# Optimization experiments

Hardware: AMD Instinct MI355X
Metric: run time of the kernel (lower is better)

The kernel has to match this reference:

```python
import jax, jax.numpy as jnp
import numpy as np


def _highway(x, Ws, bs):
    # Ws: [n_hw, 2H, H] (torch Linear layout), bs: [n_hw, 2H]
    H = x.shape[-1]
    for i in range(Ws.shape[0]):
        proj = jnp.einsum('bsh,oh->bso', x, Ws[i]) + bs[i]
        nonlin = jax.nn.relu(proj[..., :H])
        gate = jax.nn.sigmoid(proj[..., H:])
        x = gate * x + (1.0 - gate) * nonlin
    return x


def setup_inputs() -> dict:
    key = jax.random.key(0)
    ks = jax.random.split(key, 10)
    B, S, H, L, W, NHW = 32, 512, 512, 2, 4, 2
    scale = 1.0 / np.sqrt(H)
    return {
        'inputs': jax.random.normal(ks[0], (B, S, H), dtype=jnp.float32),
        'masks': jnp.ones((B, S), dtype=jnp.int32),
        'fwd_pads': jax.random.normal(ks[1], (L, W, H), dtype=jnp.float32) * scale,
        'bwd_pads': jax.random.normal(ks[2], (L, W, H), dtype=jnp.float32) * scale,
        'fwd_ws': jax.random.normal(ks[3], (L, W + 1), dtype=jnp.float32),
        'bwd_ws': jax.random.normal(ks[4], (L, W + 1), dtype=jnp.float32),
        'fwd_hw_W': jax.random.normal(ks[5], (L, NHW, 2 * H, H), dtype=jnp.float32) * scale,
        'fwd_hw_b': jax.random.normal(ks[6], (L, NHW, 2 * H), dtype=jnp.float32) * 0.1,
        'bwd_hw_W': jax.random.normal(ks[7], (L, NHW, 2 * H, H), dtype=jnp.float32) * scale,
        'bwd_hw_b': jax.random.normal(ks[8], (L, NHW, 2 * H), dtype=jnp.float32) * 0.1,
    }


def reference(inputs, masks, fwd_pads, bwd_pads, fwd_ws, bwd_ws,
              fwd_hw_W, fwd_hw_b, bwd_hw_W, bwd_hw_b):
    # inputs: [B,S,H]; masks unused (as in the torch module)
    B, S, H = inputs.shape
    L, W, _ = fwd_pads.shape
    fwd_in = inputs
    bwd_in = inputs
    outs = []
    for l in range(L):
        fp = jnp.broadcast_to(fwd_pads[l], (B, W, H))
        bp = jnp.broadcast_to(bwd_pads[l], (B, W, H))
        pf = jnp.concatenate([fp, fwd_in, bp], axis=1)  # [B, S+2W, H]
        pb = jnp.concatenate([fp, bwd_in, bp], axis=1)
        # forward window at t covers padded positions t..t+W (causal)
        f_win = jnp.stack([pf[:, k:k + S] for k in range(W + 1)], axis=0)  # [W+1,B,S,H]
        f_out = jnp.einsum('k,kbsh->bsh', fwd_ws[l], f_win)
        # backward window at t covers padded positions t+W..t+2W (anti-causal)
        b_win = jnp.stack([pb[:, W + k:W + k + S] for k in range(W + 1)], axis=0)
        b_out = jnp.einsum('k,kbsh->bsh', bwd_ws[l], b_win)
        f_out = _highway(f_out, fwd_hw_W[l], fwd_hw_b[l])
        b_out = _highway(b_out, bwd_hw_W[l], bwd_hw_b[l])
        fwd_in, bwd_in = f_out, b_out
        outs.append(jnp.concatenate([f_out, b_out], axis=-1))
    return jnp.stack(outs, axis=0)  # [L, B, S, 2H]
```

## Files before the change

kernel.cpp:

```cpp
#include <hip/hip_runtime.h>
#include <hip/hip_bf16.h>

typedef __attribute__((ext_vector_type(8))) short bf16x8;
typedef __attribute__((ext_vector_type(4))) float floatx4;

#define B_ 32
#define S_ 512
#define H_ 512
#define M_ (B_*S_)
#define K_ 512
#define N_ 1024

__device__ __forceinline__ void gload_lds16(const void* g, void* l) {
  __builtin_amdgcn_global_load_lds(
      (const __attribute__((address_space(1))) void*)g,
      (__attribute__((address_space(3))) void*)l, 16, 0, 0);
}

__global__ void cvt_kernel(const float* __restrict__ src,
                           __hip_bfloat16* __restrict__ dst, int n4) {
  int t = blockIdx.x * 256 + threadIdx.x;
  if (t >= n4) return;
  float4 v = *(const float4*)(src + (size_t)t * 4);
  union { ushort4 u; __hip_bfloat16 h[4]; } pk;
  pk.h[0] = __float2bfloat16(v.x);
  pk.h[1] = __float2bfloat16(v.y);
  pk.h[2] = __float2bfloat16(v.z);
  pk.h[3] = __float2bfloat16(v.w);
  *(ushort4*)((unsigned short*)dst + (size_t)t * 4) = pk.u;
}

__global__ void conv_kernel(const float* __restrict__ inf, const float* __restrict__ inb,
                            int instride,
                            const float* __restrict__ fpad, const float* __restrict__ bpad,
                            const float* __restrict__ fw, const float* __restrict__ bw,
                            __hip_bfloat16* __restrict__ xaf, __hip_bfloat16* __restrict__ xab) {
  int t = blockIdx.x * 256 + threadIdx.x;
  int dir = blockIdx.y;
  int row = t >> 7;
  int hv  = (t & 127) << 2;
  int s = row & (S_ - 1);
  float4 a = make_float4(0.f, 0.f, 0.f, 0.f);
  if (dir == 0) {
#pragma unroll
    for (int k = 0; k < 5; ++k) {
      float w = fw[k];
      const float* src = (s + k < 4) ? (fpad + (size_t)(s + k) * H_ + hv)
                                     : (inf + (size_t)(row + k - 4) * instride + hv);
      float4 v = *(const float4*)src;
      a.x += w * v.x; a.y += w * v.y; a.z += w * v.z; a.w += w * v.w;
    }
  } else {
#pragma unroll
    for (int k = 0; k < 5; ++k) {
      float w = bw[k];
      const float* src = (s + k < S_) ? (inb + (size_t)(row + k) * instride + hv)
                                      : (bpad + (size_t)(s + k - S_) * H_ + hv);
      float4 v = *(const float4*)src;
      a.x += w * v.x; a.y += w * v.y; a.z += w * v.z; a.w += w * v.w;
    }
  }
  __hip_bfloat16* xa = dir ? xab : xaf;
  union { ushort4 u; __hip_bfloat16 h[4]; } pk;
  pk.h[0] = __float2bfloat16(a.x);
  pk.h[1] = __float2bfloat16(a.y);
  pk.h[2] = __float2bfloat16(a.z);
  pk.h[3] = __float2bfloat16(a.w);
  *(ushort4*)((unsigned short*)xa + (size_t)row * H_ + hv) = pk.u;
}

__global__ __launch_bounds__(512, 2)
void hw_gemm(const __hip_bfloat16* __restrict__ Af, const __hip_bfloat16* __restrict__ Ab,
             const __hip_bfloat16* __restrict__ Wf, const __hip_bfloat16* __restrict__ Wb,
             const float* __restrict__ biasf, const float* __restrict__ biasb,
             __hip_bfloat16* __restrict__ Anf, __hip_bfloat16* __restrict__ Anb,
             float* __restrict__ outp, int final_mode) {
  __shared__ __align__(16) char smem[65536];

  const int tid = threadIdx.x;
  const int lane = tid & 63, wave = tid >> 6;
  const int wm = wave >> 1, wn = wave & 1;
  const int quad = lane >> 4, l16 = lane & 15;
  const int dir = blockIdx.z;

  const int n = blockIdx.x;
  const int by = n & 63, bx = n >> 6;
  const int m0 = by * 256;
  const int h0 = bx * 128;

  const __hip_bfloat16* A = dir ? Ab : Af;
  const __hip_bfloat16* Wm = dir ? Wb : Wf;
  const float* bias = dir ? biasb : biasf;
  __hip_bfloat16* An = dir ? Anb : Anf;

  floatx4 acc[4][8];
#pragma unroll
  for (int i = 0; i < 4; ++i)
#pragma unroll
    for (int j = 0; j < 8; ++j) acc[i][j] = (floatx4){0.f, 0.f, 0.f, 0.f};

  const int srow = lane >> 2;
  const int skk  = (((lane & 3) ^ ((lane >> 3) & 3)) << 3);
  const int key  = (l16 >> 1) & 3;
  const int xkp0 = bx * 4 + wn * 2;
  const int xkp1 = xkp0 + 1;

  const __hip_bfloat16* aptr[2];
  const __hip_bfloat16* bptr[2];
#pragma unroll
  for (int c = 0; c < 2; ++c) {
    const int chunk = wave * 2 + c;
    aptr[c] = A + (size_t)(m0 + chunk * 16 + srow) * K_ + skk;
    const int brow = chunk * 16 + srow;
    const int wnp = brow >> 7, rr = brow & 127;
    const int wrow = (rr < 64) ? (h0 + wnp * 64 + rr)
                               : (512 + h0 + wnp * 64 + (rr - 64));
    bptr[c] = Wm + (size_t)wrow * K_ + skk;
  }

#pragma unroll
  for (int c = 0; c < 2; ++c) {
    const int chunk = wave * 2 + c;
    gload_lds16(aptr[c], smem + chunk * 1024);
    gload_lds16(bptr[c], smem + 16384 + chunk * 1024);
  }
  __syncthreads();

  unsigned int xsp[4][4][2];
  int cur = 0;
  for (int kp = 0; kp < 16; ++kp) {
    const __hip_bfloat16* cA = (const __hip_bfloat16*)(smem + (cur << 15));
    const __hip_bfloat16* cB = (const __hip_bfloat16*)(smem + (cur << 15) + 16384);
    if (kp < 15) {
      char* nb = smem + ((cur ^ 1) << 15);
      const int kb = (kp + 1) * 32;
#pragma unroll
      for (int c = 0; c < 2; ++c) {
        const int chunk = wave * 2 + c;
        gload_lds16(aptr[c] + kb, nb + chunk * 1024);
        gload_lds16(bptr[c] + kb, nb + 16384 + chunk * 1024);
      }
    }
    if (kp == xkp0) {
      const unsigned short* pA = (const unsigned short*)cA;
#pragma unroll
      for (int i = 0; i < 4; ++i)
#pragma unroll
        for (int jj = 0; jj < 2; ++jj)
#pragma unroll
          for (int rh = 0; rh < 2; ++rh) {
            const int ra0 = wm * 64 + i * 16 + quad * 4 + rh * 2;
            const int ra1 = ra0 + 1;
            const int c2 = jj * 16 + l16;
            unsigned int lo = pA[ra0 * 32 + ((((c2 >> 3) ^ ((ra0 >> 1) & 3)) << 3) | (c2 & 7))];
            unsigned int hi = pA[ra1 * 32 + ((((c2 >> 3) ^ ((ra1 >> 1) & 3)) << 3) | (c2 & 7))];
            xsp[i][jj][rh] = lo | (hi << 16);
          }
    }
    if (kp == xkp1) {
      const unsigned short* pA = (const unsigned short*)cA;
#pragma unroll
      for (int i = 0; i < 4; ++i)
#pragma unroll
        for (int jj = 0; jj < 2; ++jj)
#pragma unroll
          for (int rh = 0; rh < 2; ++rh) {
            const int ra0 = wm * 64 + i * 16 + quad * 4 + rh * 2;
            const int ra1 = ra0 + 1;
            const int c2 = jj * 16 + l16;
            unsigned int lo = pA[ra0 * 32 + ((((c2 >> 3) ^ ((ra0 >> 1) & 3)) << 3) | (c2 & 7))];
            unsigned int hi = pA[ra1 * 32 + ((((c2 >> 3) ^ ((ra1 >> 1) & 3)) << 3) | (c2 & 7))];
            xsp[i][2 + jj][rh] = lo | (hi << 16);
          }
    }
    bf16x8 av[4];
#pragma unroll
    for (int i = 0; i < 4; ++i) {
      const int ra = wm * 64 + i * 16 + l16;
      av[i] = *(const bf16x8*)&cA[ra * 32 + ((quad ^ key) << 3)];
    }
#pragma unroll
    for (int jh = 0; jh < 2; ++jh) {
      bf16x8 bv[4];
#pragma unroll
      for (int jj = 0; jj < 4; ++jj) {
        const int rb = wn * 128 + (jh * 4 + jj) * 16 + l16;
        bv[jj] = *(const bf16x8*)&cB[rb * 32 + ((quad ^ key) << 3)];
      }
#pragma unroll
      for (int i = 0; i < 4; ++i)
#pragma unroll
        for (int jj = 0; jj < 4; ++jj)
          acc[i][jh * 4 + jj] =
              __builtin_amdgcn_mfma_f32_16x16x32_bf16(av[i], bv[jj], acc[i][jh * 4 + jj], 0, 0, 0);
    }
    __syncthreads();
    cur ^= 1;
  }

  float bnl[4], bgt[4];
#pragma unroll
  for (int j = 0; j < 4; ++j) {
    const int c = h0 + wn * 64 + j * 16 + l16;
    bnl[j] = bias[c];
    bgt[j] = bias[512 + c];
  }

  if (final_mode) {
    float* ft = (float*)smem;
#pragma unroll
    for (int p = 0; p < 2; ++p) {
      if (wn == p) {
#pragma unroll
        for (int i = 0; i < 4; ++i)
#pragma unroll
          for (int r = 0; r < 4; ++r) {
            const int rl = wm * 64 + i * 16 + quad * 4 + r;
#pragma unroll
            for (int j = 0; j < 4; ++j) {
              float pn = acc[i][j][r] + bnl[j];
              float pg = acc[i][j + 4][r] + bgt[j];
              float g = 1.f / (1.f + __expf(-pg));
              unsigned int u = xsp[i][j][r >> 1];
              unsigned int bits = (r & 1) ? (u >> 16) : (u & 0xffffu);
              float xo = __uint_as_float(bits << 16);
              ft[rl * 64 + j * 16 + l16] = g * xo + (1.f - g) * fmaxf(pn, 0.f);
            }
          }
      }
      __syncthreads();
#pragma unroll
      for (int q = 0; q < 8; ++q) {
        const int rl = q * 32 + (tid >> 4);
        const int cc = (tid & 15) * 4;
        float4 v = *(const float4*)&ft[rl * 64 + cc];
        *(float4*)&outp[(size_t)(m0 + rl) * N_ + dir * H_ + h0 + p * 64 + cc] = v;
      }
      __syncthreads();
    }
  } else {
    __hip_bfloat16* bt = (__hip_bfloat16*)smem;
#pragma unroll
    for (int i = 0; i < 4; ++i)
#pragma unroll
      for (int r = 0; r < 4; ++r) {
        const int rl = wm * 64 + i * 16 + quad * 4 + r;
#pragma unroll
        for (int j = 0; j < 4; ++j) {
          float pn = acc[i][j][r] + bnl[j];
          float pg = acc[i][j + 4][r] + bgt[j];
          float g = 1.f / (1.f + __expf(-pg));
          unsigned int u = xsp[i][j][r >> 1];
          unsigned int bits = (r & 1) ? (u >> 16) : (u & 0xffffu);
          float xo = __uint_as_float(bits << 16);
          bt[rl * 128 + wn * 64 + j * 16 + l16] =
              __float2bfloat16(g * xo + (1.f - g) * fmaxf(pn, 0.f));
        }
      }
    __syncthreads();
    const unsigned short* src = (const unsigned short*)smem;
#pragma unroll
    for (int p = 0; p < 8; ++p) {
      const int rl = p * 32 + (tid >> 4);
      const int cc = (tid & 15) * 8;
      int4 v = *(const int4*)(src + rl * 128 + cc);
      *(int4*)((unsigned short*)An + (size_t)(m0 + rl) * H_ + h0 + cc) = v;
    }
  }
}

extern "C" void kernel_launch(void* const* d_in, const int* in_sizes, int n_in,
                              void* d_out, int out_size, void* d_ws, size_t ws_size,
                              hipStream_t stream) {
  const float* inputs   = (const float*)d_in[0];
  const float* fwd_pads = (const float*)d_in[2];
  const float* bwd_pads = (const float*)d_in[3];
  const float* fwd_ws_p = (const float*)d_in[4];
  const float* bwd_ws_p = (const float*)d_in[5];
  const float* fwd_hw_W = (const float*)d_in[6];
  const float* fwd_hw_b = (const float*)d_in[7];
  const float* bwd_hw_W = (const float*)d_in[8];
  const float* bwd_hw_b = (const float*)d_in[9];
  float* out = (float*)d_out;

  char* ws = (char*)d_ws;
  size_t off = 0;
  __hip_bfloat16* Wbf = (__hip_bfloat16*)(ws + off); off += (size_t)4194304 * 2;
  __hip_bfloat16* xa0f = (__hip_bfloat16*)(ws + off); off += (size_t)M_ * H_ * 2;
  __hip_bfloat16* xa0b = (__hip_bfloat16*)(ws + off); off += (size_t)M_ * H_ * 2;
  __hip_bfloat16* xa1f = (__hip_bfloat16*)(ws + off); off += (size_t)M_ * H_ * 2;
  __hip_bfloat16* xa1b = (__hip_bfloat16*)(ws + off); off += (size_t)M_ * H_ * 2;

  cvt_kernel<<<2048, 256, 0, stream>>>(fwd_hw_W, Wbf, 524288);
  cvt_kernel<<<2048, 256, 0, stream>>>(bwd_hw_W, Wbf + (size_t)2097152, 524288);

  for (int l = 0; l < 2; ++l) {
    const float *inf, *inb;
    int instride;
    if (l == 0) { inf = inputs; inb = inputs; instride = H_; }
    else        { inf = out;    inb = out + H_; instride = N_; }
    conv_kernel<<<dim3(8192, 2), 256, 0, stream>>>(
        inf, inb, instride,
        fwd_pads + (size_t)l * 4 * H_, bwd_pads + (size_t)l * 4 * H_,
        fwd_ws_p + l * 5, bwd_ws_p + l * 5,
        xa0f, xa0b);

    hw_gemm<<<dim3(256, 1, 2), 512, 0, stream>>>(
        xa0f, xa0b,
        Wbf + (size_t)(l * 2) * 524288, Wbf + (size_t)2097152 + (size_t)(l * 2) * 524288,
        fwd_hw_b + (l * 2) * 1024, bwd_hw_b + (l * 2) * 1024,
        xa1f, xa1b, nullptr, 0);

    hw_gemm<<<dim3(256, 1, 2), 512, 0, stream>>>(
        xa1f, xa1b,
        Wbf + (size_t)(l * 2 + 1) * 524288, Wbf + (size_t)2097152 + (size_t)(l * 2 + 1) * 524288,
        fwd_hw_b + (l * 2 + 1) * 1024, bwd_hw_b + (l * 2 + 1) * 1024,
        nullptr, nullptr, out + (size_t)l * M_ * N_, 1);
  }
}
```

Baseline: 422.4 us.

## Deepen GEMM LDS prefetch pipeline with vmcnt waits and merge weight conversions

The highway GEMM now issues the first two K-slices up front and, inside the loop, waits with a partial vmcnt on the older slice instead of a full __syncthreads, then refills the just-consumed buffer two steps ahead. MFMA work is wrapped in s_setprio to favour math waves. The two weight-conversion launches are merged into one kernel. The aim is to hide global-to-LDS load latency and remove one launch, at the cost of hand-tuned waitcnt counts that must match the number of outstanding loads.

```diff
diff --git a/kernel.cpp b/kernel.cpp
--- a/kernel.cpp
+++ b/kernel.cpp
@@ -17,17 +17,21 @@
       (__attribute__((address_space(3))) void*)l, 16, 0, 0);
 }
 
-__global__ void cvt_kernel(const float* __restrict__ src,
-                           __hip_bfloat16* __restrict__ dst, int n4) {
+__global__ void cvt2_kernel(const float* __restrict__ s0, const float* __restrict__ s1,
+                            __hip_bfloat16* __restrict__ d0, __hip_bfloat16* __restrict__ d1) {
   int t = blockIdx.x * 256 + threadIdx.x;
-  if (t >= n4) return;
-  float4 v = *(const float4*)(src + (size_t)t * 4);
+  const float* src;
+  __hip_bfloat16* dst;
+  int i;
+  if (t < 524288) { src = s0; dst = d0; i = t; }
+  else            { src = s1; dst = d1; i = t - 524288; }
+  float4 v = *(const float4*)(src + (size_t)i * 4);
   union { ushort4 u; __hip_bfloat16 h[4]; } pk;
   pk.h[0] = __float2bfloat16(v.x);
   pk.h[1] = __float2bfloat16(v.y);
   pk.h[2] = __float2bfloat16(v.z);
   pk.h[3] = __float2bfloat16(v.w);
-  *(ushort4*)((unsigned short*)dst + (size_t)t * 4) = pk.u;
+  *(ushort4*)((unsigned short*)dst + (size_t)i * 4) = pk.u;
 }
 
 __global__ void conv_kernel(const float* __restrict__ inf, const float* __restrict__ inb,
@@ -124,23 +128,23 @@
     gload_lds16(aptr[c], smem + chunk * 1024);
     gload_lds16(bptr[c], smem + 16384 + chunk * 1024);
   }
-  __syncthreads();
+#pragma unroll
+  for (int c = 0; c < 2; ++c) {
+    const int chunk = wave * 2 + c;
+    gload_lds16(aptr[c] + 32, smem + 32768 + chunk * 1024);
+    gload_lds16(bptr[c] + 32, smem + 32768 + 16384 + chunk * 1024);
+  }
 
   unsigned int xsp[4][4][2];
   int cur = 0;
   for (int kp = 0; kp < 16; ++kp) {
     const __hip_bfloat16* cA = (const __hip_bfloat16*)(smem + (cur << 15));
     const __hip_bfloat16* cB = (const __hip_bfloat16*)(smem + (cur << 15) + 16384);
-    if (kp < 15) {
-      char* nb = smem + ((cur ^ 1) << 15);
-      const int kb = (kp + 1) * 32;
-#pragma unroll
-      for (int c = 0; c < 2; ++c) {
-        const int chunk = wave * 2 + c;
-        gload_lds16(aptr[c] + kb, nb + chunk * 1024);
-        gload_lds16(bptr[c] + kb, nb + 16384 + chunk * 1024);
-      }
-    }
+
+    if (kp < 15) asm volatile("s_waitcnt vmcnt(4)" ::: "memory");
+    else         asm volatile("s_waitcnt vmcnt(0)" ::: "memory");
+    __builtin_amdgcn_s_barrier();
+
     if (kp == xkp0) {
       const unsigned short* pA = (const unsigned short*)cA;
 #pragma unroll
@@ -173,6 +177,8 @@
             xsp[i][2 + jj][rh] = lo | (hi << 16);
           }
     }
+
+    __builtin_amdgcn_s_setprio(1);
     bf16x8 av[4];
 #pragma unroll
     for (int i = 0; i < 4; ++i) {
@@ -194,7 +200,21 @@
           acc[i][jh * 4 + jj] =
               __builtin_amdgcn_mfma_f32_16x16x32_bf16(av[i], bv[jj], acc[i][jh * 4 + jj], 0, 0, 0);
     }
-    __syncthreads();
+    __builtin_amdgcn_s_setprio(0);
+
+    asm volatile("s_waitcnt lgkmcnt(0)" ::: "memory");
+    __builtin_amdgcn_s_barrier();
+
+    if (kp < 14) {
+      char* nb = smem + (cur << 15);
+      const int kb = (kp + 2) * 32;
+#pragma unroll
+      for (int c = 0; c < 2; ++c) {
+        const int chunk = wave * 2 + c;
+        gload_lds16(aptr[c] + kb, nb + chunk * 1024);
+        gload_lds16(bptr[c] + kb, nb + 16384 + chunk * 1024);
+      }
+    }
     cur ^= 1;
   }
 
@@ -291,8 +311,7 @@
   __hip_bfloat16* xa1f = (__hip_bfloat16*)(ws + off); off += (size_t)M_ * H_ * 2;
   __hip_bfloat16* xa1b = (__hip_bfloat16*)(ws + off); off += (size_t)M_ * H_ * 2;
 
-  cvt_kernel<<<2048, 256, 0, stream>>>(fwd_hw_W, Wbf, 524288);
-  cvt_kernel<<<2048, 256, 0, stream>>>(bwd_hw_W, Wbf + (size_t)2097152, 524288);
+  cvt2_kernel<<<4096, 256, 0, stream>>>(fwd_hw_W, bwd_hw_W, Wbf, Wbf + (size_t)2097152);
 
   for (int l = 0; l < 2; ++l) {
     const float *inf, *inb;
```

New measurement: 428.1 us. No clear change (+1.4%).

## Use 16 waves per GEMM block with smaller per-wave tiles; merge weight conversions

Applied to the files above, without the earlier changes.

The highway GEMM block grows from 8 to 16 waves arranged 4x4. Each wave now computes a 64x64 output slice (32 nonlin + 32 gate columns) instead of 64x128, which halves the accumulator registers and the per-wave LDS load work. The per-wave global-to-LDS loads, the xsp capture and the epilogue indexing are remapped to match. The two weight-conversion launches are merged into a single kernel. In exchange, B-fragment reuse per wave is lower and there are more waves per block contending at each barrier.

```diff
diff --git a/kernel.cpp b/kernel.cpp
--- a/kernel.cpp
+++ b/kernel.cpp
@@ -17,17 +17,21 @@
       (__attribute__((address_space(3))) void*)l, 16, 0, 0);
 }
 
-__global__ void cvt_kernel(const float* __restrict__ src,
-                           __hip_bfloat16* __restrict__ dst, int n4) {
+__global__ void cvt2_kernel(const float* __restrict__ s0, const float* __restrict__ s1,
+                            __hip_bfloat16* __restrict__ d0, __hip_bfloat16* __restrict__ d1) {
   int t = blockIdx.x * 256 + threadIdx.x;
-  if (t >= n4) return;
-  float4 v = *(const float4*)(src + (size_t)t * 4);
+  const float* src;
+  __hip_bfloat16* dst;
+  int i;
+  if (t < 524288) { src = s0; dst = d0; i = t; }
+  else            { src = s1; dst = d1; i = t - 524288; }
+  float4 v = *(const float4*)(src + (size_t)i * 4);
   union { ushort4 u; __hip_bfloat16 h[4]; } pk;
   pk.h[0] = __float2bfloat16(v.x);
   pk.h[1] = __float2bfloat16(v.y);
   pk.h[2] = __float2bfloat16(v.z);
   pk.h[3] = __float2bfloat16(v.w);
-  *(ushort4*)((unsigned short*)dst + (size_t)t * 4) = pk.u;
+  *(ushort4*)((unsigned short*)dst + (size_t)i * 4) = pk.u;
 }
 
 __global__ void conv_kernel(const float* __restrict__ inf, const float* __restrict__ inb,
@@ -69,7 +73,7 @@
   *(ushort4*)((unsigned short*)xa + (size_t)row * H_ + hv) = pk.u;
 }
 
-__global__ __launch_bounds__(512, 2)
+__global__ __launch_bounds__(1024, 4)
 void hw_gemm(const __hip_bfloat16* __restrict__ Af, const __hip_bfloat16* __restrict__ Ab,
              const __hip_bfloat16* __restrict__ Wf, const __hip_bfloat16* __restrict__ Wb,
              const float* __restrict__ biasf, const float* __restrict__ biasb,
@@ -79,7 +83,7 @@
 
   const int tid = threadIdx.x;
   const int lane = tid & 63, wave = tid >> 6;
-  const int wm = wave >> 1, wn = wave & 1;
+  const int wm = wave >> 2, wn = wave & 3;
   const int quad = lane >> 4, l16 = lane & 15;
   const int dir = blockIdx.z;
 
@@ -93,40 +97,29 @@
   const float* bias = dir ? biasb : biasf;
   __hip_bfloat16* An = dir ? Anb : Anf;
 
-  floatx4 acc[4][8];
+  floatx4 acc[4][4];
 #pragma unroll
   for (int i = 0; i < 4; ++i)
 #pragma unroll
-    for (int j = 0; j < 8; ++j) acc[i][j] = (floatx4){0.f, 0.f, 0.f, 0.f};
+    for (int j = 0; j < 4; ++j) acc[i][j] = (floatx4){0.f, 0.f, 0.f, 0.f};
 
   const int srow = lane >> 2;
   const int skk  = (((lane & 3) ^ ((lane >> 3) & 3)) << 3);
   const int key  = (l16 >> 1) & 3;
-  const int xkp0 = bx * 4 + wn * 2;
-  const int xkp1 = xkp0 + 1;
-
-  const __hip_bfloat16* aptr[2];
-  const __hip_bfloat16* bptr[2];
-#pragma unroll
-  for (int c = 0; c < 2; ++c) {
-    const int chunk = wave * 2 + c;
-    aptr[c] = A + (size_t)(m0 + chunk * 16 + srow) * K_ + skk;
-    const int brow = chunk * 16 + srow;
-    const int wnp = brow >> 7, rr = brow & 127;
-    const int wrow = (rr < 64) ? (h0 + wnp * 64 + rr)
-                               : (512 + h0 + wnp * 64 + (rr - 64));
-    bptr[c] = Wm + (size_t)wrow * K_ + skk;
-  }
-
-#pragma unroll
-  for (int c = 0; c < 2; ++c) {
-    const int chunk = wave * 2 + c;
-    gload_lds16(aptr[c], smem + chunk * 1024);
-    gload_lds16(bptr[c], smem + 16384 + chunk * 1024);
-  }
+  const int xkp  = bx * 4 + wn;
+
+  const __hip_bfloat16* aptr = A + (size_t)(m0 + wave * 16 + srow) * K_ + skk;
+  const int brow = wave * 16 + srow;
+  const int wnp = brow >> 6, rr = brow & 63;
+  const int wrow = (rr < 32) ? (h0 + wnp * 32 + rr)
+                             : (512 + h0 + wnp * 32 + (rr - 32));
+  const __hip_bfloat16* bptr = Wm + (size_t)wrow * K_ + skk;
+
+  gload_lds16(aptr, smem + wave * 1024);
+  gload_lds16(bptr, smem + 16384 + wave * 1024);
   __syncthreads();
 
-  unsigned int xsp[4][4][2];
+  unsigned int xsp[4][2][2];
   int cur = 0;
   for (int kp = 0; kp < 16; ++kp) {
     const __hip_bfloat16* cA = (const __hip_bfloat16*)(smem + (cur << 15));
@@ -134,14 +127,10 @@
     if (kp < 15) {
       char* nb = smem + ((cur ^ 1) << 15);
       const int kb = (kp + 1) * 32;
-#pragma unroll
-      for (int c = 0; c < 2; ++c) {
-        const int chunk = wave * 2 + c;
-        gload_lds16(aptr[c] + kb, nb + chunk * 1024);
-        gload_lds16(bptr[c] + kb, nb + 16384 + chunk * 1024);
-      }
-    }
-    if (kp == xkp0) {
+      gload_lds16(aptr + kb, nb + wave * 1024);
+      gload_lds16(bptr + kb, nb + 16384 + wave * 1024);
+    }
+    if (kp == xkp) {
       const unsigned short* pA = (const unsigned short*)cA;
 #pragma unroll
       for (int i = 0; i < 4; ++i)
@@ -157,51 +146,31 @@
             xsp[i][jj][rh] = lo | (hi << 16);
           }
     }
-    if (kp == xkp1) {
-      const unsigned short* pA = (const unsigned short*)cA;
-#pragma unroll
-      for (int i = 0; i < 4; ++i)
-#pragma unroll
-        for (int jj = 0; jj < 2; ++jj)
-#pragma unroll
-          for (int rh = 0; rh < 2; ++rh) {
-            const int ra0 = wm * 64 + i * 16 + quad * 4 + rh * 2;
-            const int ra1 = ra0 + 1;
-            const int c2 = jj * 16 + l16;
-            unsigned int lo = pA[ra0 * 32 + ((((c2 >> 3) ^ ((ra0 >> 1) & 3)) << 3) | (c2 & 7))];
-            unsigned int hi = pA[ra1 * 32 + ((((c2 >> 3) ^ ((ra1 >> 1) & 3)) << 3) | (c2 & 7))];
-            xsp[i][2 + jj][rh] = lo | (hi << 16);
-          }
-    }
-    bf16x8 av[4];
+    bf16x8 av[4], bv[4];
 #pragma unroll
     for (int i = 0; i < 4; ++i) {
       const int ra = wm * 64 + i * 16 + l16;
       av[i] = *(const bf16x8*)&cA[ra * 32 + ((quad ^ key) << 3)];
     }
 #pragma unroll
-    for (int jh = 0; jh < 2; ++jh) {
-      bf16x8 bv[4];
-#pragma unroll
-      for (int jj = 0; jj < 4; ++jj) {
-        const int rb = wn * 128 + (jh * 4 + jj) * 16 + l16;
-        bv[jj] = *(const bf16x8*)&cB[rb * 32 + ((quad ^ key) << 3)];
-      }
-#pragma unroll
-      for (int i = 0; i < 4; ++i)
-#pragma unroll
-        for (int jj = 0; jj < 4; ++jj)
-          acc[i][jh * 4 + jj] =
-              __builtin_amdgcn_mfma_f32_16x16x32_bf16(av[i], bv[jj], acc[i][jh * 4 + jj], 0, 0, 0);
-    }
+    for (int j = 0; j < 4; ++j) {
+      const int rb = wn * 64 + j * 16 + l16;
+      bv[j] = *(const bf16x8*)&cB[rb * 32 + ((quad ^ key) << 3)];
+    }
+#pragma unroll
+    for (int i = 0; i < 4; ++i)
+#pragma unroll
+      for (int j = 0; j < 4; ++j)
+        acc[i][j] = __builtin_amdgcn_mfma_f32_16x16x32_bf16(av[i], bv[j], acc[i][j], 0, 0, 0);
+
     __syncthreads();
     cur ^= 1;
   }
 
-  float bnl[4], bgt[4];
-#pragma unroll
-  for (int j = 0; j < 4; ++j) {
-    const int c = h0 + wn * 64 + j * 16 + l16;
+  float bnl[2], bgt[2];
+#pragma unroll
+  for (int j = 0; j < 2; ++j) {
+    const int c = h0 + wn * 32 + j * 16 + l16;
     bnl[j] = bias[c];
     bgt[j] = bias[512 + c];
   }
@@ -210,28 +179,29 @@
     float* ft = (float*)smem;
 #pragma unroll
     for (int p = 0; p < 2; ++p) {
-      if (wn == p) {
+      if ((wn >> 1) == p) {
 #pragma unroll
         for (int i = 0; i < 4; ++i)
 #pragma unroll
           for (int r = 0; r < 4; ++r) {
             const int rl = wm * 64 + i * 16 + quad * 4 + r;
 #pragma unroll
-            for (int j = 0; j < 4; ++j) {
+            for (int j = 0; j < 2; ++j) {
               float pn = acc[i][j][r] + bnl[j];
-              float pg = acc[i][j + 4][r] + bgt[j];
+              float pg = acc[i][j + 2][r] + bgt[j];
               float g = 1.f / (1.f + __expf(-pg));
               unsigned int u = xsp[i][j][r >> 1];
               unsigned int bits = (r & 1) ? (u >> 16) : (u & 0xffffu);
               float xo = __uint_as_float(bits << 16);
-              ft[rl * 64 + j * 16 + l16] = g * xo + (1.f - g) * fmaxf(pn, 0.f);
+              ft[rl * 64 + (wn & 1) * 32 + j * 16 + l16] =
+                  g * xo + (1.f - g) * fmaxf(pn, 0.f);
             }
           }
       }
       __syncthreads();
 #pragma unroll
-      for (int q = 0; q < 8; ++q) {
-        const int rl = q * 32 + (tid >> 4);
+      for (int q = 0; q < 4; ++q) {
+        const int rl = q * 64 + (tid >> 4);
         const int cc = (tid & 15) * 4;
         float4 v = *(const float4*)&ft[rl * 64 + cc];
         *(float4*)&outp[(size_t)(m0 + rl) * N_ + dir * H_ + h0 + p * 64 + cc] = v;
@@ -246,22 +216,22 @@
       for (int r = 0; r < 4; ++r) {
         const int rl = wm * 64 + i * 16 + quad * 4 + r;
 #pragma unroll
-        for (int j = 0; j < 4; ++j) {
+        for (int j = 0; j < 2; ++j) {
           float pn = acc[i][j][r] + bnl[j];
-          float pg = acc[i][j + 4][r] + bgt[j];
+          float pg = acc[i][j + 2][r] + bgt[j];
           float g = 1.f / (1.f + __expf(-pg));
           unsigned int u = xsp[i][j][r >> 1];
           unsigned int bits = (r & 1) ? (u >> 16) : (u & 0xffffu);
           float xo = __uint_as_float(bits << 16);
-          bt[rl * 128 + wn * 64 + j * 16 + l16] =
+          bt[rl * 128 + wn * 32 + j * 16 + l16] =
               __float2bfloat16(g * xo + (1.f - g) * fmaxf(pn, 0.f));
         }
       }
     __syncthreads();
     const unsigned short* src = (const unsigned short*)smem;
 #pragma unroll
-    for (int p = 0; p < 8; ++p) {
-      const int rl = p * 32 + (tid >> 4);
+    for (int q = 0; q < 4; ++q) {
+      const int rl = q * 64 + (tid >> 4);
       const int cc = (tid & 15) * 8;
       int4 v = *(const int4*)(src + rl * 128 + cc);
       *(int4*)((unsigned short*)An + (size_t)(m0 + rl) * H_ + h0 + cc) = v;
@@ -291,8 +261,7 @@
   __hip_bfloat16* xa1f = (__hip_bfloat16*)(ws + off); off += (size_t)M_ * H_ * 2;
   __hip_bfloat16* xa1b = (__hip_bfloat16*)(ws + off); off += (size_t)M_ * H_ * 2;
 
-  cvt_kernel<<<2048, 256, 0, stream>>>(fwd_hw_W, Wbf, 524288);
-  cvt_kernel<<<2048, 256, 0, stream>>>(bwd_hw_W, Wbf + (size_t)2097152, 524288);
+  cvt2_kernel<<<4096, 256, 0, stream>>>(fwd_hw_W, bwd_hw_W, Wbf, Wbf + (size_t)2097152);
 
   for (int l = 0; l < 2; ++l) {
     const float *inf, *inb;
@@ -305,13 +274,13 @@
         fwd_ws_p + l * 5, bwd_ws_p + l * 5,
         xa0f, xa0b);
 
-    hw_gemm<<<dim3(256, 1, 2), 512, 0, stream>>>(
+    hw_gemm<<<dim3(256, 1, 2), 1024, 0, stream>>>(
         xa0f, xa0b,
         Wbf + (size_t)(l * 2) * 524288, Wbf + (size_t)2097152 + (size_t)(l * 2) * 524288,
         fwd_hw_b + (l * 2) * 1024, bwd_hw_b + (l * 2) * 1024,
         xa1f, xa1b, nullptr, 0);
 
-    hw_gemm<<<dim3(256, 1, 2), 512, 0, stream>>>(
+    hw_gemm<<<dim3(256, 1, 2), 1024, 0, stream>>>(
         xa1f, xa1b,
         Wbf + (size_t)(l * 2 + 1) * 524288, Wbf + (size_t)2097152 + (size_t)(l * 2 + 1) * 524288,
         fwd_hw_b + (l * 2 + 1) * 1024, bwd_hw_b + (l * 2 + 1) * 1024,
```

New measurement: 460.7 us. 9.1% more time.
